# Performance work log

Hardware: AMD Instinct MI355X
Metric: run time of the kernel (lower is better)

## Reference

```python
import jax, jax.numpy as jnp
import numpy as np

B = 4096
D0, D1 = 256, 64


def setup_inputs() -> dict:
    key = jax.random.key(0)
    k0, k1, k2, k3 = jax.random.split(key, 4)
    return {
        "s0": jax.random.normal(k0, (B, D0), dtype=jnp.float32),
        "s1": jax.random.normal(k1, (B, D1), dtype=jnp.float32),
        "t0": jax.random.normal(k2, (B, D0), dtype=jnp.float32),
        "t1": jax.random.normal(k3, (B, D1), dtype=jnp.float32),
    }


def _gaussian_kernel(source, target):
    # feats: [2B, D]
    feats = jnp.concatenate([source, target], axis=0)
    n = feats.shape[0]
    # pairwise squared distances [2B, 2B] via the Gram-matrix identity
    # (same math as ((x - y) ** 2).sum(-1), avoids the [N, N, D] intermediate)
    sq = jnp.sum(feats * feats, axis=-1)
    dist = sq[:, None] + sq[None, :] - 2.0 * (feats @ feats.T)
    # median-heuristic bandwidth with num_kernels=1: gamma = (n^2 - n) / sum(dist)
    gamma = (n * n - n) / jnp.sum(jax.lax.stop_gradient(dist))
    return jnp.exp(-dist * gamma)


def reference(s0, s1, t0, t1):
    # joint kernel: elementwise product of per-stream Gaussian kernels
    k = _gaussian_kernel(s0, t0) * _gaussian_kernel(s1, t1)
    b = s0.shape[0]
    s2s = k[:b, :b]
    t2t = k[b:, b:]
    s2t = k[:b, b:]
    return jnp.mean(s2s + t2t - 2.0 * s2t)
```

## Files before the change

### kernel.cpp

```cpp
#include <hip/hip_runtime.h>
#include <hip/hip_fp8.h>

#define B_ROWS 4096
#define NTOT   8192
#define D0     256
#define D1     64
#define KDIM   320
#define NSB    128
#define NTILE  64
#define NTRI   2080

typedef __attribute__((ext_vector_type(4))) float f32x4;
typedef __attribute__((ext_vector_type(2))) long long2v;

#define OFF_GAM   0
#define OFF_PQ0   32
#define OFF_PQ1   544
#define OFF_P0    1056
#define OFF_P1    132128
#define OFF_R     164896
#define OFF_BSUM  197664
#define OFF_PHI   214304

__device__ __forceinline__ void load_lds16(const void* g, void* l) {
    __builtin_amdgcn_global_load_lds(
        (const __attribute__((address_space(1))) void*)g,
        (__attribute__((address_space(3))) void*)l, 16, 0, 0);
}

__global__ __launch_bounds__(256) void k_stats(
    const float* __restrict__ s0, const float* __restrict__ s1,
    const float* __restrict__ t0, const float* __restrict__ t1,
    float* __restrict__ part0, float* __restrict__ part1,
    float* __restrict__ pq0, float* __restrict__ pq1) {
    __shared__ float sh0[4][256];
    __shared__ float sh1[4][64];
    __shared__ float shq[4][2];
    int t = threadIdx.x, wv = t >> 6, lane = t & 63;
    int rb = blockIdx.x * 64;
    int c4 = lane * 4;
    int rr = wv;

    f32x4 cs = {0.f, 0.f, 0.f, 0.f};
    float q0 = 0.f;
    #pragma unroll 4
    for (int k = 0; k < 16; ++k) {
        int row = rb + rr + k * 4;
        const float* b0 = (row < B_ROWS) ? s0 + (size_t)row * D0 : t0 + (size_t)(row - B_ROWS) * D0;
        f32x4 v = *(const f32x4*)(b0 + c4);
        cs.x += v.x; cs.y += v.y; cs.z += v.z; cs.w += v.w;
        q0 += v.x * v.x + v.y * v.y + v.z * v.z + v.w * v.w;
    }
    *(f32x4*)&sh0[rr][c4] = cs;

    float cs1 = 0.f, q1 = 0.f;
    #pragma unroll 4
    for (int k = 0; k < 16; ++k) {
        int row = rb + rr + k * 4;
        const float* b1 = (row < B_ROWS) ? s1 + (size_t)row * D1 : t1 + (size_t)(row - B_ROWS) * D1;
        float v = b1[lane];
        cs1 += v; q1 += v * v;
    }
    sh1[rr][lane] = cs1;

    #pragma unroll
    for (int o = 32; o; o >>= 1) { q0 += __shfl_xor(q0, o, 64); q1 += __shfl_xor(q1, o, 64); }
    if (lane == 0) { shq[wv][0] = q0; shq[wv][1] = q1; }
    __syncthreads();

    part0[blockIdx.x * D0 + t] = sh0[0][t] + sh0[1][t] + sh0[2][t] + sh0[3][t];
    if (t < D1) part1[blockIdx.x * D1 + t] = sh1[0][t] + sh1[1][t] + sh1[2][t] + sh1[3][t];
    if (t == 0) {
        pq0[blockIdx.x] = shq[0][0] + shq[1][0] + shq[2][0] + shq[3][0];
        pq1[blockIdx.x] = shq[0][1] + shq[1][1] + shq[2][1] + shq[3][1];
    }
}

__global__ __launch_bounds__(256) void k_gamma(
    const float* __restrict__ pq0, const float* __restrict__ pq1,
    const float* __restrict__ part0, const float* __restrict__ part1,
    float* __restrict__ gam) {
    __shared__ double sh[4][4];
    int t = threadIdx.x, wv = t >> 6, lane = t & 63;

    double a0 = 0.0, a1 = 0.0;
    if (t < NSB) { a0 = (double)pq0[t]; a1 = (double)pq1[t]; }

    double F0t = 0.0;
    for (int b = 0; b < NSB; ++b) F0t += (double)part0[b * D0 + t];
    double nf0 = F0t * F0t;

    double nf1 = 0.0;
    if (t < D1) {
        double F1t = 0.0;
        for (int b = 0; b < NSB; ++b) F1t += (double)part1[b * D1 + t];
        nf1 = F1t * F1t;
    }

    #pragma unroll
    for (int o = 32; o; o >>= 1) {
        a0  += __shfl_xor(a0, o, 64);
        a1  += __shfl_xor(a1, o, 64);
        nf0 += __shfl_xor(nf0, o, 64);
        nf1 += __shfl_xor(nf1, o, 64);
    }
    if (lane == 0) { sh[wv][0] = a0; sh[wv][1] = a1; sh[wv][2] = nf0; sh[wv][3] = nf1; }
    __syncthreads();
    if (t == 0) {
        double b0 = 0, b1 = 0, b2 = 0, b3 = 0;
        for (int w = 0; w < 4; ++w) { b0 += sh[w][0]; b1 += sh[w][1]; b2 += sh[w][2]; b3 += sh[w][3]; }
        double n = (double)NTOT;
        double g0 = (n * n - n) / (2.0 * n * b0 - 2.0 * b2);
        double g1 = (n * n - n) / (2.0 * n * b1 - 2.0 * b3);
        gam[0] = (float)g0; gam[1] = (float)g1;
        gam[2] = (float)sqrt(g0); gam[3] = (float)sqrt(g1);
    }
}

__global__ __launch_bounds__(256) void k_pack(
    const float* __restrict__ s0, const float* __restrict__ s1,
    const float* __restrict__ t0, const float* __restrict__ t1,
    const float* __restrict__ gam, unsigned char* __restrict__ phi,
    float* __restrict__ rvec) {
    int wv = threadIdx.x >> 6, lane = threadIdx.x & 63;
    int row = blockIdx.x * 4 + wv;
    float sg0 = gam[2], sg1 = gam[3];
    const float* b0 = (row < B_ROWS) ? s0 + (size_t)row * D0 : t0 + (size_t)(row - B_ROWS) * D0;
    const float* b1 = (row < B_ROWS) ? s1 + (size_t)row * D1 : t1 + (size_t)(row - B_ROWS) * D1;
    unsigned char* pr = phi + (size_t)row * KDIM;
    f32x4 v = *(const f32x4*)(b0 + lane * 4);
    __hip_fp8_e4m3 q0(v.x * sg0), q1(v.y * sg0), q2(v.z * sg0), q3(v.w * sg0);
    unsigned int word = (unsigned int)q0.__x | ((unsigned int)q1.__x << 8) |
                        ((unsigned int)q2.__x << 16) | ((unsigned int)q3.__x << 24);
    int doff0 = ((lane >> 4) << 6) + (((lane >> 1) & 3) << 4) +
                (((lane >> 3) & 1) << 3) + ((lane & 1) << 2);
    *(unsigned int*)(pr + doff0) = word;
    float f0 = (float)q0, f1 = (float)q1, f2 = (float)q2, f3 = (float)q3;
    float p = f0 * f0 + f1 * f1 + f2 * f2 + f3 * f3;
    __hip_fp8_e4m3 qd(b1[lane] * sg1);
    int doff1 = 256 + (((lane >> 3) & 3) << 4) + (((lane >> 5) & 1) << 3) + (lane & 7);
    pr[doff1] = qd.__x;
    float fd = (float)qd;
    p += fd * fd;
    #pragma unroll
    for (int o = 32; o; o >>= 1) p += __shfl_xor(p, o, 64);
    if (lane == 0) rvec[row] = p;
}

__global__ __launch_bounds__(256, 2) void k_mmd(
    const unsigned char* __restrict__ phi, const float* __restrict__ rvec,
    double* __restrict__ blocksum) {
    int tb = (blockIdx.x & 7) * (NTRI / 8) + (blockIdx.x >> 3);
    int I = (int)((129.0f - sqrtf(16641.0f - 8.0f * (float)tb)) * 0.5f);
    while ((129 * I - I * I) / 2 > tb) --I;
    while ((129 * (I + 1) - (I + 1) * (I + 1)) / 2 <= tb) ++I;
    int J = I + (tb - (129 * I - I * I) / 2);

    __shared__ unsigned char As[40960];
    __shared__ unsigned char Bs[40960];

    int tid = threadIdx.x, wv = tid >> 6, lane = tid & 63;
    int wr = wv >> 1, wc = wv & 1;
    int rgrp = lane >> 4, rlow = lane & 15;
    int wvb = wv * 1024;
    const int rowA = I * 128, rowB = J * 128;

    f32x4 acc_[4][4] = {};

    #pragma unroll
    for (int c = 0; c < 5; ++c) {
        #pragma unroll
        for (int it = 0; it < 2; ++it) {
            int u = it * 256 + tid;
            int row = u >> 2, sl = u & 3;
            int rg = sl ^ ((row >> 1) & 3);
            size_t gcol = (size_t)c * 64 + rg * 16;
            load_lds16(phi + (size_t)(rowA + row) * KDIM + gcol,
                       As + c * 8192 + it * 4096 + wvb);
            load_lds16(phi + (size_t)(rowB + row) * KDIM + gcol,
                       Bs + c * 8192 + it * 4096 + wvb);
        }
    }
    __syncthreads();

    #pragma unroll
    for (int tt = 0; tt < 5; ++tt) {
        long2v af[4], bf[4];
        #pragma unroll
        for (int m = 0; m < 4; ++m) {
            int row = wr * 64 + m * 16 + rlow;
            int sl = rgrp ^ ((row >> 1) & 3);
            af[m] = *(const long2v*)&As[tt * 8192 + row * 64 + sl * 16];
        }
        #pragma unroll
        for (int n = 0; n < 4; ++n) {
            int col = wc * 64 + n * 16 + rlow;
            int sl = rgrp ^ ((col >> 1) & 3);
            bf[n] = *(const long2v*)&Bs[tt * 8192 + col * 64 + sl * 16];
        }
        __builtin_amdgcn_s_setprio(1);
        #pragma unroll
        for (int m = 0; m < 4; ++m)
            #pragma unroll
            for (int n = 0; n < 4; ++n) {
                acc_[m][n] = __builtin_amdgcn_mfma_f32_16x16x32_fp8_fp8(
                    af[m][0], bf[n][0], acc_[m][n], 0, 0, 0);
                acc_[m][n] = __builtin_amdgcn_mfma_f32_16x16x32_fp8_fp8(
                    af[m][1], bf[n][1], acc_[m][n], 0, 0, 0);
            }
        __builtin_amdgcn_s_setprio(0);
    }

    float psum = 0.f;
    #pragma unroll
    for (int m = 0; m < 4; ++m) {
        f32x4 ri = *(const f32x4*)&rvec[rowA + wr * 64 + m * 16 + rgrp * 4];
        #pragma unroll
        for (int n = 0; n < 4; ++n) {
            float rj = rvec[rowB + wc * 64 + n * 16 + rlow];
            f32x4 a = acc_[m][n];
            psum += __expf(2.f * a.x - ri.x - rj);
            psum += __expf(2.f * a.y - ri.y - rj);
            psum += __expf(2.f * a.z - ri.z - rj);
            psum += __expf(2.f * a.w - ri.w - rj);
        }
    }
    #pragma unroll
    for (int o = 32; o; o >>= 1) psum += __shfl_xor(psum, o, 64);

    __syncthreads();
    float* ws = (float*)As;
    if (lane == 0) ws[wv] = psum;
    __syncthreads();
    if (tid == 0) {
        float bs = ws[0] + ws[1] + ws[2] + ws[3];
        double sgn = ((I < 32) == (J < 32)) ? 1.0 : -1.0;
        double fac = (I == J) ? 1.0 : 2.0;
        blocksum[tb] = sgn * fac * (double)bs;
    }
}

__global__ __launch_bounds__(256) void k_final(
    const double* __restrict__ blocksum, float* __restrict__ out) {
    __shared__ double sh[4];
    int t = threadIdx.x, wv = t >> 6, lane = t & 63;
    double s = 0.0;
    for (int i = t; i < NTRI; i += 256) s += blocksum[i];
    #pragma unroll
    for (int o = 32; o; o >>= 1) s += __shfl_xor(s, o, 64);
    if (lane == 0) sh[wv] = s;
    __syncthreads();
    if (t == 0) {
        double tot = sh[0] + sh[1] + sh[2] + sh[3];
        out[0] = (float)(tot / ((double)B_ROWS * (double)B_ROWS));
    }
}

extern "C" void kernel_launch(void* const* d_in, const int* in_sizes, int n_in,
                              void* d_out, int out_size, void* d_ws, size_t ws_size,
                              hipStream_t stream) {
    const float* s0 = (const float*)d_in[0];
    const float* s1 = (const float*)d_in[1];
    const float* t0 = (const float*)d_in[2];
    const float* t1 = (const float*)d_in[3];
    char* ws = (char*)d_ws;
    float*  gam  = (float*)(ws + OFF_GAM);
    float*  pq0  = (float*)(ws + OFF_PQ0);
    float*  pq1  = (float*)(ws + OFF_PQ1);
    float*  p0   = (float*)(ws + OFF_P0);
    float*  p1   = (float*)(ws + OFF_P1);
    float*  rvec = (float*)(ws + OFF_R);
    double* bsum = (double*)(ws + OFF_BSUM);
    unsigned char* phi = (unsigned char*)(ws + OFF_PHI);

    k_stats<<<NSB, 256, 0, stream>>>(s0, s1, t0, t1, p0, p1, pq0, pq1);
    k_gamma<<<1, 256, 0, stream>>>(pq0, pq1, p0, p1, gam);
    k_pack<<<2048, 256, 0, stream>>>(s0, s1, t0, t1, gam, phi, rvec);
    k_mmd<<<NTRI, 256, 0, stream>>>(phi, rvec, bsum);
    k_final<<<1, 256, 0, stream>>>(bsum, (float*)d_out);
}
```

Before: 55.83 us.

## Fuse fp8 packing into stats kernel, apply gamma scaling inside MMD kernel

Removes the separate pack kernel. Inputs are quantised to fp8 without gamma scaling inside the stats pass, so packing no longer has to wait for gamma. The MMD kernel keeps separate squared norms per stream and combines the two partial Gram products with a gamma ratio before the exponential. LDS use is cut by staging the K dimension in two phases (3 tiles then 2), which allows 3 blocks per CU. The cost is an extra barrier-separated load phase and an fp8 rounding difference because quantisation now happens before scaling.

Measured after the change: 57.43 us. 2.9% more time.

```diff
diff --git a/kernel.cpp b/kernel.cpp
--- a/kernel.cpp
+++ b/kernel.cpp
@@ -18,9 +18,10 @@
 #define OFF_PQ1   544
 #define OFF_P0    1056
 #define OFF_P1    132128
-#define OFF_R     164896
-#define OFF_BSUM  197664
-#define OFF_PHI   214304
+#define OFF_R0    164896
+#define OFF_R1    197664
+#define OFF_BSUM  230432
+#define OFF_PHI   247072
 
 __device__ __forceinline__ void load_lds16(const void* g, void* l) {
     __builtin_amdgcn_global_load_lds(
@@ -28,11 +29,13 @@
         (__attribute__((address_space(3))) void*)l, 16, 0, 0);
 }
 
-__global__ __launch_bounds__(256) void k_stats(
+__global__ __launch_bounds__(256) void k_prep(
     const float* __restrict__ s0, const float* __restrict__ s1,
     const float* __restrict__ t0, const float* __restrict__ t1,
     float* __restrict__ part0, float* __restrict__ part1,
-    float* __restrict__ pq0, float* __restrict__ pq1) {
+    float* __restrict__ pq0, float* __restrict__ pq1,
+    unsigned char* __restrict__ phi,
+    float* __restrict__ r0vec, float* __restrict__ r1vec) {
     __shared__ float sh0[4][256];
     __shared__ float sh1[4][64];
     __shared__ float shq[4][2];
@@ -74,6 +77,32 @@
         pq0[blockIdx.x] = shq[0][0] + shq[1][0] + shq[2][0] + shq[3][0];
         pq1[blockIdx.x] = shq[0][1] + shq[1][1] + shq[2][1] + shq[3][1];
     }
+
+    for (int r = 0; r < 16; ++r) {
+        int row = rb + wv * 16 + r;
+        const float* b0p = (row < B_ROWS) ? s0 + (size_t)row * D0
+                                          : t0 + (size_t)(row - B_ROWS) * D0;
+        const float* b1p = (row < B_ROWS) ? s1 + (size_t)row * D1
+                                          : t1 + (size_t)(row - B_ROWS) * D1;
+        unsigned char* pr = phi + (size_t)row * KDIM;
+        f32x4 v = *(const f32x4*)(b0p + lane * 4);
+        __hip_fp8_e4m3 a0(v.x), a1(v.y), a2(v.z), a3(v.w);
+        unsigned int word = (unsigned int)a0.__x | ((unsigned int)a1.__x << 8) |
+                            ((unsigned int)a2.__x << 16) | ((unsigned int)a3.__x << 24);
+        int doff0 = ((lane >> 4) << 6) + (((lane >> 1) & 3) << 4) +
+                    (((lane >> 3) & 1) << 3) + ((lane & 1) << 2);
+        *(unsigned int*)(pr + doff0) = word;
+        float f0 = (float)a0, f1 = (float)a1, f2 = (float)a2, f3 = (float)a3;
+        float p0 = f0 * f0 + f1 * f1 + f2 * f2 + f3 * f3;
+        __hip_fp8_e4m3 qd(b1p[lane]);
+        int doff1 = 256 + (((lane >> 3) & 3) << 4) + (((lane >> 5) & 1) << 3) + (lane & 7);
+        pr[doff1] = qd.__x;
+        float fd = (float)qd;
+        float p1 = fd * fd;
+        #pragma unroll
+        for (int o = 32; o; o >>= 1) { p0 += __shfl_xor(p0, o, 64); p1 += __shfl_xor(p1, o, 64); }
+        if (lane == 0) { r0vec[row] = p0; r1vec[row] = p1; }
+    }
 }
 
 __global__ __launch_bounds__(256) void k_gamma(
@@ -113,91 +142,67 @@
         double g0 = (n * n - n) / (2.0 * n * b0 - 2.0 * b2);
         double g1 = (n * n - n) / (2.0 * n * b1 - 2.0 * b3);
         gam[0] = (float)g0; gam[1] = (float)g1;
-        gam[2] = (float)sqrt(g0); gam[3] = (float)sqrt(g1);
-    }
-}
-
-__global__ __launch_bounds__(256) void k_pack(
-    const float* __restrict__ s0, const float* __restrict__ s1,
-    const float* __restrict__ t0, const float* __restrict__ t1,
-    const float* __restrict__ gam, unsigned char* __restrict__ phi,
-    float* __restrict__ rvec) {
-    int wv = threadIdx.x >> 6, lane = threadIdx.x & 63;
-    int row = blockIdx.x * 4 + wv;
-    float sg0 = gam[2], sg1 = gam[3];
-    const float* b0 = (row < B_ROWS) ? s0 + (size_t)row * D0 : t0 + (size_t)(row - B_ROWS) * D0;
-    const float* b1 = (row < B_ROWS) ? s1 + (size_t)row * D1 : t1 + (size_t)(row - B_ROWS) * D1;
-    unsigned char* pr = phi + (size_t)row * KDIM;
-    f32x4 v = *(const f32x4*)(b0 + lane * 4);
-    __hip_fp8_e4m3 q0(v.x * sg0), q1(v.y * sg0), q2(v.z * sg0), q3(v.w * sg0);
-    unsigned int word = (unsigned int)q0.__x | ((unsigned int)q1.__x << 8) |
-                        ((unsigned int)q2.__x << 16) | ((unsigned int)q3.__x << 24);
-    int doff0 = ((lane >> 4) << 6) + (((lane >> 1) & 3) << 4) +
-                (((lane >> 3) & 1) << 3) + ((lane & 1) << 2);
-    *(unsigned int*)(pr + doff0) = word;
-    float f0 = (float)q0, f1 = (float)q1, f2 = (float)q2, f3 = (float)q3;
-    float p = f0 * f0 + f1 * f1 + f2 * f2 + f3 * f3;
-    __hip_fp8_e4m3 qd(b1[lane] * sg1);
-    int doff1 = 256 + (((lane >> 3) & 3) << 4) + (((lane >> 5) & 1) << 3) + (lane & 7);
-    pr[doff1] = qd.__x;
-    float fd = (float)qd;
-    p += fd * fd;
-    #pragma unroll
-    for (int o = 32; o; o >>= 1) p += __shfl_xor(p, o, 64);
-    if (lane == 0) rvec[row] = p;
-}
-
-__global__ __launch_bounds__(256, 2) void k_mmd(
-    const unsigned char* __restrict__ phi, const float* __restrict__ rvec,
-    double* __restrict__ blocksum) {
+        gam[2] = (float)(g1 / g0); gam[3] = (float)(2.0 * g0);
+    }
+}
+
+__global__ __launch_bounds__(256, 3) void k_mmd(
+    const unsigned char* __restrict__ phi,
+    const float* __restrict__ r0vec, const float* __restrict__ r1vec,
+    const float* __restrict__ gam, double* __restrict__ blocksum) {
     int tb = (blockIdx.x & 7) * (NTRI / 8) + (blockIdx.x >> 3);
     int I = (int)((129.0f - sqrtf(16641.0f - 8.0f * (float)tb)) * 0.5f);
     while ((129 * I - I * I) / 2 > tb) --I;
     while ((129 * (I + 1) - (I + 1) * (I + 1)) / 2 <= tb) ++I;
     int J = I + (tb - (129 * I - I * I) / 2);
 
-    __shared__ unsigned char As[40960];
-    __shared__ unsigned char Bs[40960];
+    __shared__ unsigned char As[24576];
+    __shared__ unsigned char Bs[24576];
+    __shared__ float wsum[4];
 
     int tid = threadIdx.x, wv = tid >> 6, lane = tid & 63;
     int wr = wv >> 1, wc = wv & 1;
     int rgrp = lane >> 4, rlow = lane & 15;
-    int wvb = wv * 1024;
     const int rowA = I * 128, rowB = J * 128;
 
+    const float g0 = gam[0], g1 = gam[1], ratio = gam[2], tg0 = gam[3];
+
     f32x4 acc_[4][4] = {};
 
-    #pragma unroll
-    for (int c = 0; c < 5; ++c) {
-        #pragma unroll
-        for (int it = 0; it < 2; ++it) {
-            int u = it * 256 + tid;
-            int row = u >> 2, sl = u & 3;
-            int rg = sl ^ ((row >> 1) & 3);
-            size_t gcol = (size_t)c * 64 + rg * 16;
-            load_lds16(phi + (size_t)(rowA + row) * KDIM + gcol,
-                       As + c * 8192 + it * 4096 + wvb);
-            load_lds16(phi + (size_t)(rowB + row) * KDIM + gcol,
-                       Bs + c * 8192 + it * 4096 + wvb);
+    #define STAGE(tbase, nt)                                                    \
+        _Pragma("unroll")                                                       \
+        for (int it = 0; it < (nt) * 2; ++it) {                                 \
+            int idx = it * 256 + tid;                                           \
+            int tt = idx >> 9, rs = idx & 511;                                  \
+            int row = rs >> 2, slot = rs & 3;                                   \
+            int rg = slot ^ ((row >> 1) & 3);                                   \
+            size_t gcol = ((tbase) + tt) * 64 + rg * 16;                        \
+            load_lds16(phi + (size_t)(rowA + row) * KDIM + gcol,                \
+                       As + it * 4096 + wv * 1024);                             \
+            load_lds16(phi + (size_t)(rowB + row) * KDIM + gcol,                \
+                       Bs + it * 4096 + wv * 1024);                             \
         }
-    }
-    __syncthreads();
-
-    #pragma unroll
-    for (int tt = 0; tt < 5; ++tt) {
-        long2v af[4], bf[4];
-        #pragma unroll
-        for (int m = 0; m < 4; ++m) {
-            int row = wr * 64 + m * 16 + rlow;
-            int sl = rgrp ^ ((row >> 1) & 3);
-            af[m] = *(const long2v*)&As[tt * 8192 + row * 64 + sl * 16];
+
+    #define LOADFRAG(tt)                                                        \
+        long2v af[4], bf[4];                                                    \
+        _Pragma("unroll")                                                       \
+        for (int m = 0; m < 4; ++m) {                                           \
+            int row = wr * 64 + m * 16 + rlow;                                  \
+            int sl = rgrp ^ ((row >> 1) & 3);                                   \
+            af[m] = *(const long2v*)&As[(tt) * 8192 + row * 64 + sl * 16];      \
+        }                                                                       \
+        _Pragma("unroll")                                                       \
+        for (int n = 0; n < 4; ++n) {                                           \
+            int col = wc * 64 + n * 16 + rlow;                                  \
+            int sl = rgrp ^ ((col >> 1) & 3);                                   \
+            bf[n] = *(const long2v*)&Bs[(tt) * 8192 + col * 64 + sl * 16];      \
         }
-        #pragma unroll
-        for (int n = 0; n < 4; ++n) {
-            int col = wc * 64 + n * 16 + rlow;
-            int sl = rgrp ^ ((col >> 1) & 3);
-            bf[n] = *(const long2v*)&Bs[tt * 8192 + col * 64 + sl * 16];
-        }
+
+    STAGE(0, 3);
+    __syncthreads();
+    #pragma unroll
+    for (int tt = 0; tt < 3; ++tt) {
+        LOADFRAG(tt);
         __builtin_amdgcn_s_setprio(1);
         #pragma unroll
         for (int m = 0; m < 4; ++m)
@@ -210,30 +215,64 @@
             }
         __builtin_amdgcn_s_setprio(0);
     }
+    __syncthreads();
+    STAGE(3, 2);
+    __syncthreads();
+    {
+        LOADFRAG(0);
+        __builtin_amdgcn_s_setprio(1);
+        #pragma unroll
+        for (int m = 0; m < 4; ++m)
+            #pragma unroll
+            for (int n = 0; n < 4; ++n) {
+                acc_[m][n] = __builtin_amdgcn_mfma_f32_16x16x32_fp8_fp8(
+                    af[m][0], bf[n][0], acc_[m][n], 0, 0, 0);
+                acc_[m][n] = __builtin_amdgcn_mfma_f32_16x16x32_fp8_fp8(
+                    af[m][1], bf[n][1], acc_[m][n], 0, 0, 0);
+            }
+        __builtin_amdgcn_s_setprio(0);
+    }
+    {
+        LOADFRAG(1);
+        __builtin_amdgcn_s_setprio(1);
+        #pragma unroll
+        for (int m = 0; m < 4; ++m)
+            #pragma unroll
+            for (int n = 0; n < 4; ++n) {
+                f32x4 tm = {0.f, 0.f, 0.f, 0.f};
+                tm = __builtin_amdgcn_mfma_f32_16x16x32_fp8_fp8(
+                    af[m][0], bf[n][0], tm, 0, 0, 0);
+                tm = __builtin_amdgcn_mfma_f32_16x16x32_fp8_fp8(
+                    af[m][1], bf[n][1], tm, 0, 0, 0);
+                acc_[m][n] += ratio * tm;
+            }
+        __builtin_amdgcn_s_setprio(0);
+    }
 
     float psum = 0.f;
     #pragma unroll
     for (int m = 0; m < 4; ++m) {
-        f32x4 ri = *(const f32x4*)&rvec[rowA + wr * 64 + m * 16 + rgrp * 4];
+        int gi = rowA + wr * 64 + m * 16 + rgrp * 4;
+        f32x4 r0i = *(const f32x4*)&r0vec[gi];
+        f32x4 r1i = *(const f32x4*)&r1vec[gi];
+        f32x4 ui = g0 * r0i + g1 * r1i;
         #pragma unroll
         for (int n = 0; n < 4; ++n) {
-            float rj = rvec[rowB + wc * 64 + n * 16 + rlow];
+            int gj = rowB + wc * 64 + n * 16 + rlow;
+            float uj = g0 * r0vec[gj] + g1 * r1vec[gj];
             f32x4 a = acc_[m][n];
-            psum += __expf(2.f * a.x - ri.x - rj);
-            psum += __expf(2.f * a.y - ri.y - rj);
-            psum += __expf(2.f * a.z - ri.z - rj);
-            psum += __expf(2.f * a.w - ri.w - rj);
+            psum += __expf(tg0 * a.x - ui.x - uj);
+            psum += __expf(tg0 * a.y - ui.y - uj);
+            psum += __expf(tg0 * a.z - ui.z - uj);
+            psum += __expf(tg0 * a.w - ui.w - uj);
         }
     }
     #pragma unroll
     for (int o = 32; o; o >>= 1) psum += __shfl_xor(psum, o, 64);
-
-    __syncthreads();
-    float* ws = (float*)As;
-    if (lane == 0) ws[wv] = psum;
+    if (lane == 0) wsum[wv] = psum;
     __syncthreads();
     if (tid == 0) {
-        float bs = ws[0] + ws[1] + ws[2] + ws[3];
+        float bs = wsum[0] + wsum[1] + wsum[2] + wsum[3];
         double sgn = ((I < 32) == (J < 32)) ? 1.0 : -1.0;
         double fac = (I == J) ? 1.0 : 2.0;
         blocksum[tb] = sgn * fac * (double)bs;
@@ -269,13 +308,13 @@
     float*  pq1  = (float*)(ws + OFF_PQ1);
     float*  p0   = (float*)(ws + OFF_P0);
     float*  p1   = (float*)(ws + OFF_P1);
-    float*  rvec = (float*)(ws + OFF_R);
+    float*  r0v  = (float*)(ws + OFF_R0);
+    float*  r1v  = (float*)(ws + OFF_R1);
     double* bsum = (double*)(ws + OFF_BSUM);
     unsigned char* phi = (unsigned char*)(ws + OFF_PHI);
 
-    k_stats<<<NSB, 256, 0, stream>>>(s0, s1, t0, t1, p0, p1, pq0, pq1);
+    k_prep<<<NSB, 256, 0, stream>>>(s0, s1, t0, t1, p0, p1, pq0, pq1, phi, r0v, r1v);
     k_gamma<<<1, 256, 0, stream>>>(pq0, pq1, p0, p1, gam);
-    k_pack<<<2048, 256, 0, stream>>>(s0, s1, t0, t1, gam, phi, rvec);
-    k_mmd<<<NTRI, 256, 0, stream>>>(phi, rvec, bsum);
+    k_mmd<<<NTRI, 256, 0, stream>>>(phi, r0v, r1v, gam, bsum);
     k_final<<<1, 256, 0, stream>>>(bsum, (float*)d_out);
 }
```
